# Optimization experiments

Measured on AMD Instinct MI355X. Metric: run time of the kernel, lower is better.

The kernel has to match this reference:

```python
import jax, jax.numpy as jnp
import numpy as np

N = 100000       # nodes
E = 1600000      # edges (avg degree 16)
F_IN = 128       # num_features
H = 128          # hidden
C = 10           # num_classes
L = 3            # num_layers
G = 128          # number of graphs in the batch


def setup_inputs() -> dict:
    key = jax.random.key(0)
    ks = jax.random.split(key, 12)
    x = jax.random.normal(ks[0], (N, F_IN), dtype=jnp.float32)
    edge_index = jax.random.randint(ks[1], (2, E), 0, N, dtype=jnp.int64)
    batch = jnp.sort(jax.random.randint(ks[2], (N,), 0, G, dtype=jnp.int64))
    def lin(k, fan_in, fan_out):
        s = 1.0 / np.sqrt(fan_in)
        return jax.random.uniform(k, (fan_in, fan_out), jnp.float32, -s, s)
    w_init = lin(ks[3], F_IN, H)
    b_init = jnp.zeros((H,), jnp.float32)
    w_conv = jnp.stack([lin(ks[4 + i], H, H) for i in range(L - 1)])  # [L-1,H,H]
    b_conv = jnp.zeros((L - 1, H), jnp.float32)
    w_h1 = lin(ks[8], H, H)
    b_h1 = jnp.zeros((H,), jnp.float32)
    w_h2 = lin(ks[9], H, C)
    b_h2 = jnp.zeros((C,), jnp.float32)
    return {"x": x, "edge_index": edge_index, "batch": batch,
            "w_init": w_init, "b_init": b_init,
            "w_conv": w_conv, "b_conv": b_conv,
            "w_h1": w_h1, "b_h1": b_h1, "w_h2": w_h2, "b_h2": b_h2}


def reference(x, edge_index, batch, w_init, b_init, w_conv, b_conv,
              w_h1, b_h1, w_h2, b_h2):
    n = x.shape[0]
    # GCNConv normalization: add self-loops, symmetric deg^-1/2 norm.
    loop = jnp.arange(n, dtype=edge_index.dtype)
    src = jnp.concatenate([edge_index[0], loop])
    dst = jnp.concatenate([edge_index[1], loop])
    deg = jax.ops.segment_sum(jnp.ones_like(dst, x.dtype), dst, num_segments=n)
    dinv = jnp.where(deg > 0, jax.lax.rsqrt(deg), 0.0)
    norm = dinv[src] * dinv[dst]  # [E+N]

    def gcn_conv(h, w, b):
        h = h @ w                                   # [N,H]
        msg = norm[:, None] * h[src]                # gather + scale
        return jax.ops.segment_sum(msg, dst, num_segments=n) + b

    h = jax.nn.relu(gcn_conv(x, w_init, b_init))
    for i in range(w_conv.shape[0]):
        h = jax.nn.relu(gcn_conv(h, w_conv[i], b_conv[i]))

    # global_mean_pool over graph ids
    sums = jax.ops.segment_sum(h, batch, num_segments=G)           # [G,H]
    cnt = jax.ops.segment_sum(jnp.ones((n,), h.dtype), batch, num_segments=G)
    pooled = sums / jnp.maximum(cnt, 1.0)[:, None]

    # classification head (dropout = identity at inference)
    h = jax.nn.relu(pooled @ w_h1 + b_h1)
    logits = h @ w_h2 + b_h2
    return jax.nn.log_softmax(logits, axis=-1)
```

## Files before the change

kernel.cpp:

```cpp
#include <hip/hip_runtime.h>
#include <hip/hip_bf16.h>
#include <math.h>

#define NN 100000
#define EE 1600000
#define HD 128
#define GG 128
#define CC 10

#define BKSH 9
#define NBK  196
#define CH   4096
#define MAXB 12288

typedef __attribute__((ext_vector_type(8))) short short8;
typedef __attribute__((ext_vector_type(4))) float f32x4;
typedef __attribute__((ext_vector_type(2))) float f32x2;

__device__ __forceinline__ unsigned short f2bf(float f) {
    union { float f; unsigned u; } a; a.f = f;
    unsigned r = a.u + 0x7fff + ((a.u >> 16) & 1);
    return (unsigned short)(r >> 16);
}
__device__ __forceinline__ float bfu(unsigned short u) {
    union { unsigned u; float f; } a; a.u = ((unsigned)u) << 16; return a.f;
}

__device__ __forceinline__ unsigned pk4fp8(float f0, float f1, float f2, float f3) {
    unsigned u = 0;
    u = __builtin_amdgcn_cvt_pk_fp8_f32(f0, f1, u, false);
    u = __builtin_amdgcn_cvt_pk_fp8_f32(f2, f3, u, true);
    return u;
}


__global__ __launch_bounds__(256) void k_bhist(const int* __restrict__ dst,
                                               unsigned* __restrict__ bucket_cnt) {
    __shared__ unsigned cnt[256];
    int t = threadIdx.x;
    cnt[t] = 0;
    __syncthreads();
    int base = blockIdx.x * CH;
#pragma unroll
    for (int k = 0; k < 16; ++k) {
        int e = base + k * 256 + t;
        if (e < EE) atomicAdd(&cnt[((unsigned)dst[e]) >> BKSH], 1u);
    }
    __syncthreads();
    if (cnt[t]) atomicAdd(&bucket_cnt[t], cnt[t]);
}

__global__ void k_bscan(const unsigned* __restrict__ bucket_cnt,
                        unsigned* __restrict__ bucket_start,
                        unsigned* __restrict__ cursor, int* __restrict__ row_start) {
    __shared__ unsigned s[256];
    int t = threadIdx.x;
    unsigned v = bucket_cnt[t];
    s[t] = v;
    __syncthreads();
    for (int off = 1; off < 256; off <<= 1) {
        unsigned a = (t >= off) ? s[t - off] : 0;
        __syncthreads();
        s[t] += a;
        __syncthreads();
    }
    unsigned excl = s[t] - v;
    bucket_start[t] = excl;
    cursor[t] = excl;
    if (t == 255) bucket_start[256] = excl + v;
    if (t == 0) row_start[NN] = EE;
}

__global__ __launch_bounds__(256) void k_bscatter(const int* __restrict__ src,
                                                  const int* __restrict__ dst,
                                                  unsigned* __restrict__ cursor,
                                                  unsigned* __restrict__ ebuf) {
    __shared__ unsigned cnt[256], lst[256], gbase[256], ss[256];
    __shared__ unsigned stage[CH];
    __shared__ unsigned char binid[CH];
    int t = threadIdx.x;
    cnt[t] = 0;
    __syncthreads();
    int base = blockIdx.x * CH;
    int nvalid = EE - base; if (nvalid > CH) nvalid = CH;

    unsigned bk[16], rk[16], pv[16];
#pragma unroll
    for (int k = 0; k < 16; ++k) {
        int e = base + k * 256 + t;
        bk[k] = 0xffffffffu;
        if (e < EE) {
            unsigned d = (unsigned)dst[e];
            unsigned b = d >> BKSH;
            pv[k] = (((unsigned)src[e]) << BKSH) | (d & ((1u << BKSH) - 1));
            bk[k] = b;
            rk[k] = atomicAdd(&cnt[b], 1u);
        }
    }
    __syncthreads();
    unsigned v = cnt[t];
    ss[t] = v;
    __syncthreads();
    for (int off = 1; off < 256; off <<= 1) {
        unsigned a = (t >= off) ? ss[t - off] : 0;
        __syncthreads();
        ss[t] += a;
        __syncthreads();
    }
    lst[t] = ss[t] - v;
    if (v) gbase[t] = atomicAdd(&cursor[t], v);
    __syncthreads();
#pragma unroll
    for (int k = 0; k < 16; ++k) {
        if (bk[k] != 0xffffffffu) {
            unsigned slot = lst[bk[k]] + rk[k];
            stage[slot] = pv[k];
            binid[slot] = (unsigned char)bk[k];
        }
    }
    __syncthreads();
    for (int j = t; j < nvalid; j += 256) {
        unsigned b = binid[j];
        ebuf[gbase[b] + (j - lst[b])] = stage[j];
    }
}

__global__ __launch_bounds__(512) void k_bucket_csr(const unsigned* __restrict__ ebuf,
                                                    const unsigned* __restrict__ bucket_start,
                                                    int* __restrict__ row_start,
                                                    float* __restrict__ dinv,
                                                    int* __restrict__ col) {
    __shared__ unsigned degl[512], lst[512], lfill[512], ss[512];
    __shared__ int colstage[MAXB];
    int t = threadIdx.x, b = blockIdx.x;
    unsigned ebase = bucket_start[b];
    int size = (int)(bucket_start[b + 1] - ebase);
    int nbase = b << BKSH;
    degl[t] = 0;
    lfill[t] = 0;
    __syncthreads();
    for (int j = t; j < size; j += 512)
        atomicAdd(&degl[ebuf[ebase + j] & 511u], 1u);
    __syncthreads();
    unsigned v = degl[t];
    ss[t] = v;
    __syncthreads();
    for (int off = 1; off < 512; off <<= 1) {
        unsigned a = (t >= off) ? ss[t - off] : 0;
        __syncthreads();
        ss[t] += a;
        __syncthreads();
    }
    lst[t] = ss[t] - v;
    int node = nbase + t;
    if (node < NN) {
        row_start[node] = (int)(ebase + lst[t]);
        dinv[node] = rsqrtf((float)(v + 1));
    }
    __syncthreads();
    if (size <= MAXB) {
        for (int j = t; j < size; j += 512) {
            unsigned u = ebuf[ebase + j];
            unsigned l = u & 511u;
            unsigned pos = lst[l] + atomicAdd(&lfill[l], 1u);
            colstage[pos] = (int)(u >> BKSH);
        }
        __syncthreads();
        for (int j = t; j < size; j += 512) col[ebase + j] = colstage[j];
    } else {
        for (int j = t; j < size; j += 512) {
            unsigned u = ebuf[ebase + j];
            unsigned l = u & 511u;
            unsigned pos = lst[l] + atomicAdd(&lfill[l], 1u);
            col[ebase + pos] = (int)(u >> BKSH);
        }
    }
}


__global__ void k_prep_w(const float* __restrict__ w0, const float* __restrict__ w1,
                         const float* __restrict__ w2, unsigned short* __restrict__ Wt) {
    int b = blockIdx.x;
    int mat = b >> 6;
    int idx = (b & 63) * 256 + threadIdx.x;
    int k = idx >> 7, n = idx & 127;
    const float* Wm = (mat == 0) ? w0 : ((mat == 1) ? w1 : w2);
    Wt[mat * 16384 + n * 128 + k] = f2bf(Wm[k * 128 + n]);
}


#define LDK 136

template <bool F32IN>
__global__ __launch_bounds__(256) void k_gemm_mfma(
    const void* __restrict__ Ap, const unsigned short* __restrict__ Wt,
    const float* __restrict__ dinv, unsigned* __restrict__ g8) {
    __shared__ unsigned short As[128 * LDK];
    __shared__ unsigned short Ws[128 * LDK];
    __shared__ float dv[128];
    int t = threadIdx.x;
    int r0 = blockIdx.x * 128;

#pragma unroll
    for (int p = 0; p < 8; ++p) {
        int chunk = p * 256 + t;
        int row = chunk >> 4, kc = chunk & 15;
        uint4 sv = make_uint4(0u, 0u, 0u, 0u);
        if (F32IN) {
            const float* A = (const float*)Ap;
            if (r0 + row < NN) {
                const float* ap = A + (size_t)(r0 + row) * HD + kc * 8;
                float4 va = *(const float4*)ap;
                float4 vb = *(const float4*)(ap + 4);
                sv.x = (unsigned)f2bf(va.x) | ((unsigned)f2bf(va.y) << 16);
                sv.y = (unsigned)f2bf(va.z) | ((unsigned)f2bf(va.w) << 16);
                sv.z = (unsigned)f2bf(vb.x) | ((unsigned)f2bf(vb.y) << 16);
                sv.w = (unsigned)f2bf(vb.z) | ((unsigned)f2bf(vb.w) << 16);
            }
        } else {
            const unsigned short* A = (const unsigned short*)Ap;
            if (r0 + row < NN) sv = *(const uint4*)(A + (size_t)(r0 + row) * HD + kc * 8);
        }
        *(uint4*)(As + row * LDK + kc * 8) = sv;
        uint4 w = *(const uint4*)(Wt + (size_t)row * HD + kc * 8);
        *(uint4*)(Ws + row * LDK + kc * 8) = w;
    }
    if (t < 128) dv[t] = (r0 + t < NN) ? dinv[r0 + t] : 0.f;
    __syncthreads();

    int wave = t >> 6, lane = t & 63, quad = lane >> 4, l16 = lane & 15;
    int wr = (wave >> 1) * 64, wc = (wave & 1) * 64;

    f32x4 acc[4][4];
#pragma unroll
    for (int i = 0; i < 4; ++i)
#pragma unroll
        for (int j = 0; j < 4; ++j) acc[i][j] = (f32x4){0.f, 0.f, 0.f, 0.f};

#pragma unroll
    for (int kk = 0; kk < 4; ++kk) {
        int k0 = kk * 32 + quad * 8;
        short8 af[4], bfr[4];
#pragma unroll
        for (int i = 0; i < 4; ++i)
            af[i] = *(const short8*)(As + (wr + i * 16 + l16) * LDK + k0);
#pragma unroll
        for (int j = 0; j < 4; ++j)
            bfr[j] = *(const short8*)(Ws + (wc + j * 16 + l16) * LDK + k0);
#pragma unroll
        for (int i = 0; i < 4; ++i)
#pragma unroll
            for (int j = 0; j < 4; ++j)
                acc[i][j] = __builtin_amdgcn_mfma_f32_16x16x32_bf16(af[i], bfr[j], acc[i][j], 0, 0, 0);
    }
    __syncthreads();

#pragma unroll
    for (int i = 0; i < 4; ++i) {
        int lr = wr + i * 16 + quad * 4;
#pragma unroll
        for (int reg = 0; reg < 4; ++reg) {
            float sc = dv[lr + reg];
#pragma unroll
            for (int j = 0; j < 4; ++j)
                As[(lr + reg) * LDK + wc + j * 16 + l16] = f2bf(acc[i][j][reg] * sc);
        }
    }
    __syncthreads();

    int row = t >> 1, half = t & 1;
    if (r0 + row < NN) {
        const unsigned short* sp = As + row * LDK + half * 64;
        unsigned og[16];
#pragma unroll
        for (int q = 0; q < 16; ++q)
            og[q] = pk4fp8(bfu(sp[4 * q]), bfu(sp[4 * q + 1]),
                           bfu(sp[4 * q + 2]), bfu(sp[4 * q + 3]));
        uint4* dp = (uint4*)(g8 + (size_t)(r0 + row) * 32 + half * 16);
#pragma unroll
        for (int q = 0; q < 4; ++q)
            dp[q] = make_uint4(og[4 * q], og[4 * q + 1], og[4 * q + 2], og[4 * q + 3]);
    }
}


__global__ __launch_bounds__(256) void k_aggregate(
    const unsigned* __restrict__ g8, const int* __restrict__ row_start,
    const int* __restrict__ col, const float* __restrict__ dinv,
    const float* __restrict__ bias, uint2* __restrict__ out) {
    int node = blockIdx.x * 8 + (threadIdx.x >> 5);
    int l = threadIdx.x & 31;
    unsigned su = g8[node * 32 + l];
    f32x2 slo = __builtin_amdgcn_cvt_pk_f32_fp8(su, false);
    f32x2 shi = __builtin_amdgcn_cvt_pk_f32_fp8(su, true);
    float a0 = slo.x, a1 = slo.y, a2 = shi.x, a3 = shi.y;
    int e = row_start[node], end = row_start[node + 1];
    for (; e + 8 <= end; e += 8) {
        int s0 = col[e], s1 = col[e + 1], s2 = col[e + 2], s3 = col[e + 3];
        int s4 = col[e + 4], s5 = col[e + 5], s6 = col[e + 6], s7 = col[e + 7];
        unsigned u0 = g8[s0 * 32 + l];
        unsigned u1 = g8[s1 * 32 + l];
        unsigned u2 = g8[s2 * 32 + l];
        unsigned u3 = g8[s3 * 32 + l];
        unsigned u4 = g8[s4 * 32 + l];
        unsigned u5 = g8[s5 * 32 + l];
        unsigned u6 = g8[s6 * 32 + l];
        unsigned u7 = g8[s7 * 32 + l];
#pragma unroll
        for (int k = 0; k < 8; ++k) {
            unsigned u = (k == 0) ? u0 : (k == 1) ? u1 : (k == 2) ? u2 : (k == 3) ? u3
                       : (k == 4) ? u4 : (k == 5) ? u5 : (k == 6) ? u6 : u7;
            f32x2 lo = __builtin_amdgcn_cvt_pk_f32_fp8(u, false);
            f32x2 hi = __builtin_amdgcn_cvt_pk_f32_fp8(u, true);
            a0 += lo.x; a1 += lo.y; a2 += hi.x; a3 += hi.y;
        }
    }
    for (; e < end; ++e) {
        unsigned u = g8[col[e] * 32 + l];
        f32x2 lo = __builtin_amdgcn_cvt_pk_f32_fp8(u, false);
        f32x2 hi = __builtin_amdgcn_cvt_pk_f32_fp8(u, true);
        a0 += lo.x; a1 += lo.y; a2 += hi.x; a3 += hi.y;
    }
    float sc = dinv[node];
    float4 bb = ((const float4*)bias)[l];
    float r0 = fmaxf(fmaf(a0, sc, bb.x), 0.f);
    float r1 = fmaxf(fmaf(a1, sc, bb.y), 0.f);
    float r2 = fmaxf(fmaf(a2, sc, bb.z), 0.f);
    float r3 = fmaxf(fmaf(a3, sc, bb.w), 0.f);
    uint2 o;
    o.x = (unsigned)f2bf(r0) | ((unsigned)f2bf(r1) << 16);
    o.y = (unsigned)f2bf(r2) | ((unsigned)f2bf(r3) << 16);
    out[node * 32 + l] = o;
}


__global__ __launch_bounds__(256) void k_pool_partial(
    const unsigned short* __restrict__ h, const int* __restrict__ batch,
    float* __restrict__ pooled, float* __restrict__ cntg) {
    int t = threadIdx.x;
    int slot = t >> 7, feat = t & 127;
    int base = blockIdx.x * 128;
    int endr = base + 128; if (endr > NN) endr = NN;
    float acc = 0.f;
    int cur = -1, run = 0;
    for (int r = base + slot; r < endr; r += 2) {
        int g = batch[r];
        float v = bfu(h[(size_t)r * HD + feat]);
        if (g != cur) {
            if (cur >= 0) {
                atomicAdd(&pooled[cur * HD + feat], acc);
                if (feat == 0) atomicAdd(&cntg[cur], (float)run);
            }
            cur = g; acc = 0.f; run = 0;
        }
        acc += v; ++run;
    }
    if (cur >= 0) {
        atomicAdd(&pooled[cur * HD + feat], acc);
        if (feat == 0) atomicAdd(&cntg[cur], (float)run);
    }
}


__global__ __launch_bounds__(128) void k_head(const float* __restrict__ pooled,
                                              const float* __restrict__ cntg,
                                              const float* __restrict__ w1,
                                              const float* __restrict__ b1,
                                              const float* __restrict__ w2,
                                              const float* __restrict__ b2,
                                              float* __restrict__ out) {
    __shared__ float row[HD], hrow[HD], logits[CC];
    int g = blockIdx.x, t = threadIdx.x;
    row[t] = pooled[g * HD + t] / fmaxf(cntg[g], 1.f);
    __syncthreads();
    float acc = b1[t];
    for (int k = 0; k < HD; ++k) acc = fmaf(row[k], w1[k * HD + t], acc);
    hrow[t] = fmaxf(acc, 0.f);
    __syncthreads();
    if (t < CC) {
        float a = b2[t];
        for (int k = 0; k < HD; ++k) a = fmaf(hrow[k], w2[k * CC + t], a);
        logits[t] = a;
    }
    __syncthreads();
    if (t < CC) {
        float m = logits[0];
        for (int i = 1; i < CC; ++i) m = fmaxf(m, logits[i]);
        float s = 0.f;
        for (int i = 0; i < CC; ++i) s += expf(logits[i] - m);
        out[g * CC + t] = logits[t] - m - logf(s);
    }
}


extern "C" void kernel_launch(void* const* d_in, const int* in_sizes, int n_in,
                              void* d_out, int out_size, void* d_ws, size_t ws_size,
                              hipStream_t stream) {
    const float* x      = (const float*)d_in[0];
    const int*   ei     = (const int*)d_in[1];
    const int*   batch  = (const int*)d_in[2];
    const float* w_init = (const float*)d_in[3];
    const float* b_init = (const float*)d_in[4];
    const float* w_conv = (const float*)d_in[5];
    const float* b_conv = (const float*)d_in[6];
    const float* w_h1   = (const float*)d_in[7];
    const float* b_h1   = (const float*)d_in[8];
    const float* w_h2   = (const float*)d_in[9];
    const float* b_h2   = (const float*)d_in[10];
    float* out = (float*)d_out;
    (void)n_in; (void)in_sizes; (void)out_size; (void)ws_size;

    char* ws = (char*)d_ws;
    size_t off = 0;
    auto alloc = [&](size_t bytes) -> void* {
        void* p = ws + off;
        off += (bytes + 255) & ~(size_t)255;
        return p;
    };
    unsigned short* hAbf         = (unsigned short*)alloc((size_t)NN * HD * 2);
    unsigned*       g8           = (unsigned*)alloc((size_t)NN * 32 * 4);
    unsigned short* Wt           = (unsigned short*)alloc(3 * 16384 * 2);
    float*          dinv         = (float*)alloc((size_t)NN * 4);
    int*            row_start    = (int*)alloc((size_t)(NN + 1) * 4);
    int*            col          = (int*)alloc((size_t)EE * 4);
    unsigned*       ebuf         = (unsigned*)alloc((size_t)EE * 4);
    unsigned*       bucket_cnt   = (unsigned*)alloc(256 * 4);
    unsigned*       bucket_start = (unsigned*)alloc(257 * 4);
    unsigned*       cursor       = (unsigned*)alloc(256 * 4);
    float*          pooled       = (float*)alloc((size_t)GG * HD * 4);
    float*          cntg         = (float*)alloc((size_t)GG * 4);

    const int* srcp = ei;
    const int* dstp = ei + EE;

    hipMemsetAsync(bucket_cnt, 0, 256 * 4, stream);
    hipMemsetAsync(pooled, 0, (size_t)GG * HD * 4, stream);
    hipMemsetAsync(cntg, 0, (size_t)GG * 4, stream);

    int nchunks = (EE + CH - 1) / CH;
    k_bhist<<<nchunks, 256, 0, stream>>>(dstp, bucket_cnt);
    k_bscan<<<1, 256, 0, stream>>>(bucket_cnt, bucket_start, cursor, row_start);
    k_bscatter<<<nchunks, 256, 0, stream>>>(srcp, dstp, cursor, ebuf);
    k_bucket_csr<<<NBK, 512, 0, stream>>>(ebuf, bucket_start, row_start, dinv, col);

    k_prep_w<<<192, 256, 0, stream>>>(w_init, w_conv, w_conv + HD * HD, Wt);

    int gemm_grid = (NN + 127) / 128;
    int agg_grid = NN / 8;

    k_gemm_mfma<true><<<gemm_grid, 256, 0, stream>>>(x, Wt, dinv, g8);
    k_aggregate<<<agg_grid, 256, 0, stream>>>(g8, row_start, col, dinv, b_init, (uint2*)hAbf);
    k_gemm_mfma<false><<<gemm_grid, 256, 0, stream>>>(hAbf, Wt + 16384, dinv, g8);
    k_aggregate<<<agg_grid, 256, 0, stream>>>(g8, row_start, col, dinv, b_conv, (uint2*)hAbf);
    k_gemm_mfma<false><<<gemm_grid, 256, 0, stream>>>(hAbf, Wt + 2 * 16384, dinv, g8);
    k_aggregate<<<agg_grid, 256, 0, stream>>>(g8, row_start, col, dinv, b_conv + HD, (uint2*)hAbf);

    k_pool_partial<<<(NN + 127) / 128, 256, 0, stream>>>(hAbf, batch, pooled, cntg);
    k_head<<<GG, 128, 0, stream>>>(pooled, cntg, w_h1, b_h1, w_h2, b_h2, out);
}
```

Before: 379.5 us.

## Fuse aggregation with next layer's GEMM and replace memsets with init kernel

Result: slower. 428.0 us (+12.8%).

```diff
diff --git a/kernel.cpp b/kernel.cpp
--- a/kernel.cpp
+++ b/kernel.cpp
@@ -31,6 +31,16 @@
     u = __builtin_amdgcn_cvt_pk_fp8_f32(f0, f1, u, false);
     u = __builtin_amdgcn_cvt_pk_fp8_f32(f2, f3, u, true);
     return u;
+}
+
+
+__global__ __launch_bounds__(256) void k_init(unsigned* __restrict__ bucket_cnt,
+                                              float* __restrict__ pooled,
+                                              float* __restrict__ cntg) {
+    int t = threadIdx.x;
+    bucket_cnt[t] = 0;
+    for (int i = t; i < GG * HD; i += 256) pooled[i] = 0.f;
+    if (t < GG) cntg[t] = 0.f;
 }
 
 
@@ -191,9 +201,8 @@
 
 #define LDK 136
 
-template <bool F32IN>
 __global__ __launch_bounds__(256) void k_gemm_mfma(
-    const void* __restrict__ Ap, const unsigned short* __restrict__ Wt,
+    const float* __restrict__ A, const unsigned short* __restrict__ Wt,
     const float* __restrict__ dinv, unsigned* __restrict__ g8) {
     __shared__ unsigned short As[128 * LDK];
     __shared__ unsigned short Ws[128 * LDK];
@@ -206,20 +215,14 @@
         int chunk = p * 256 + t;
         int row = chunk >> 4, kc = chunk & 15;
         uint4 sv = make_uint4(0u, 0u, 0u, 0u);
-        if (F32IN) {
-            const float* A = (const float*)Ap;
-            if (r0 + row < NN) {
-                const float* ap = A + (size_t)(r0 + row) * HD + kc * 8;
-                float4 va = *(const float4*)ap;
-                float4 vb = *(const float4*)(ap + 4);
-                sv.x = (unsigned)f2bf(va.x) | ((unsigned)f2bf(va.y) << 16);
-                sv.y = (unsigned)f2bf(va.z) | ((unsigned)f2bf(va.w) << 16);
-                sv.z = (unsigned)f2bf(vb.x) | ((unsigned)f2bf(vb.y) << 16);
-                sv.w = (unsigned)f2bf(vb.z) | ((unsigned)f2bf(vb.w) << 16);
-            }
-        } else {
-            const unsigned short* A = (const unsigned short*)Ap;
-            if (r0 + row < NN) sv = *(const uint4*)(A + (size_t)(r0 + row) * HD + kc * 8);
+        if (r0 + row < NN) {
+            const float* ap = A + (size_t)(r0 + row) * HD + kc * 8;
+            float4 va = *(const float4*)ap;
+            float4 vb = *(const float4*)(ap + 4);
+            sv.x = (unsigned)f2bf(va.x) | ((unsigned)f2bf(va.y) << 16);
+            sv.y = (unsigned)f2bf(va.z) | ((unsigned)f2bf(va.w) << 16);
+            sv.z = (unsigned)f2bf(vb.x) | ((unsigned)f2bf(vb.y) << 16);
+            sv.w = (unsigned)f2bf(vb.z) | ((unsigned)f2bf(vb.w) << 16);
         }
         *(uint4*)(As + row * LDK + kc * 8) = sv;
         uint4 w = *(const uint4*)(Wt + (size_t)row * HD + kc * 8);
@@ -280,6 +283,116 @@
 #pragma unroll
         for (int q = 0; q < 4; ++q)
             dp[q] = make_uint4(og[4 * q], og[4 * q + 1], og[4 * q + 2], og[4 * q + 3]);
+    }
+}
+
+
+__global__ __launch_bounds__(256) void k_agg_gemm(
+    const unsigned* __restrict__ g8in, const int* __restrict__ row_start,
+    const int* __restrict__ col, const float* __restrict__ dinv,
+    const float* __restrict__ bias, const unsigned short* __restrict__ Wt,
+    unsigned* __restrict__ g8out) {
+    __shared__ unsigned short As[64 * LDK];
+    __shared__ float dv[64];
+    int t = threadIdx.x;
+    int r0 = blockIdx.x * 64;
+    if (t < 64) dv[t] = (r0 + t < NN) ? dinv[r0 + t] : 0.f;
+
+    int h = t >> 5, l = t & 31;
+    float4 bb = ((const float4*)bias)[l];
+
+    for (int p = 0; p < 8; ++p) {
+        int row = h * 8 + p;
+        int node = r0 + row;
+        unsigned lo_u = 0, hi_u = 0;
+        if (node < NN) {
+            unsigned su = g8in[node * 32 + l];
+            f32x2 a01 = __builtin_amdgcn_cvt_pk_f32_fp8(su, false);
+            f32x2 a23 = __builtin_amdgcn_cvt_pk_f32_fp8(su, true);
+            int e = row_start[node], end = row_start[node + 1];
+            for (; e + 8 <= end; e += 8) {
+                int s0 = col[e], s1 = col[e + 1], s2 = col[e + 2], s3 = col[e + 3];
+                int s4 = col[e + 4], s5 = col[e + 5], s6 = col[e + 6], s7 = col[e + 7];
+                unsigned u0 = g8in[s0 * 32 + l];
+                unsigned u1 = g8in[s1 * 32 + l];
+                unsigned u2 = g8in[s2 * 32 + l];
+                unsigned u3 = g8in[s3 * 32 + l];
+                unsigned u4 = g8in[s4 * 32 + l];
+                unsigned u5 = g8in[s5 * 32 + l];
+                unsigned u6 = g8in[s6 * 32 + l];
+                unsigned u7 = g8in[s7 * 32 + l];
+#pragma unroll
+                for (int k = 0; k < 8; ++k) {
+                    unsigned u = (k == 0) ? u0 : (k == 1) ? u1 : (k == 2) ? u2 : (k == 3) ? u3
+                               : (k == 4) ? u4 : (k == 5) ? u5 : (k == 6) ? u6 : u7;
+                    a01 += __builtin_amdgcn_cvt_pk_f32_fp8(u, false);
+                    a23 += __builtin_amdgcn_cvt_pk_f32_fp8(u, true);
+                }
+            }
+            for (; e < end; ++e) {
+                unsigned u = g8in[col[e] * 32 + l];
+                a01 += __builtin_amdgcn_cvt_pk_f32_fp8(u, false);
+                a23 += __builtin_amdgcn_cvt_pk_f32_fp8(u, true);
+            }
+            float sc = dinv[node];
+            float r0f = fmaxf(fmaf(a01.x, sc, bb.x), 0.f);
+            float r1f = fmaxf(fmaf(a01.y, sc, bb.y), 0.f);
+            float r2f = fmaxf(fmaf(a23.x, sc, bb.z), 0.f);
+            float r3f = fmaxf(fmaf(a23.y, sc, bb.w), 0.f);
+            lo_u = (unsigned)f2bf(r0f) | ((unsigned)f2bf(r1f) << 16);
+            hi_u = (unsigned)f2bf(r2f) | ((unsigned)f2bf(r3f) << 16);
+        }
+        *(uint2*)(As + row * LDK + 4 * l) = make_uint2(lo_u, hi_u);
+    }
+    __syncthreads();
+
+    int wave = t >> 6, lane = t & 63, quad = lane >> 4, l16 = lane & 15;
+    f32x4 acc[4][2];
+#pragma unroll
+    for (int i = 0; i < 4; ++i)
+#pragma unroll
+        for (int j = 0; j < 2; ++j) acc[i][j] = (f32x4){0.f, 0.f, 0.f, 0.f};
+
+#pragma unroll
+    for (int kk = 0; kk < 4; ++kk) {
+        int k0 = kk * 32 + quad * 8;
+        short8 af[4];
+#pragma unroll
+        for (int i = 0; i < 4; ++i)
+            af[i] = *(const short8*)(As + (i * 16 + l16) * LDK + k0);
+        short8 b0 = *(const short8*)(Wt + (size_t)(wave * 32 + l16) * HD + k0);
+        short8 b1 = *(const short8*)(Wt + (size_t)(wave * 32 + 16 + l16) * HD + k0);
+#pragma unroll
+        for (int i = 0; i < 4; ++i) {
+            acc[i][0] = __builtin_amdgcn_mfma_f32_16x16x32_bf16(af[i], b0, acc[i][0], 0, 0, 0);
+            acc[i][1] = __builtin_amdgcn_mfma_f32_16x16x32_bf16(af[i], b1, acc[i][1], 0, 0, 0);
+        }
+    }
+    __syncthreads();
+
+#pragma unroll
+    for (int i = 0; i < 4; ++i) {
+        int lr = i * 16 + quad * 4;
+#pragma unroll
+        for (int reg = 0; reg < 4; ++reg) {
+            float sc = dv[lr + reg];
+            As[(lr + reg) * LDK + wave * 32 + l16] = f2bf(acc[i][0][reg] * sc);
+            As[(lr + reg) * LDK + wave * 32 + 16 + l16] = f2bf(acc[i][1][reg] * sc);
+        }
+    }
+    __syncthreads();
+
+    int row = t >> 2, seg = t & 3;
+    if (r0 + row < NN) {
+        const unsigned short* sp = As + row * LDK + seg * 32;
+        unsigned og[8];
+#pragma unroll
+        for (int q = 0; q < 8; ++q)
+            og[q] = pk4fp8(bfu(sp[4 * q]), bfu(sp[4 * q + 1]),
+                           bfu(sp[4 * q + 2]), bfu(sp[4 * q + 3]));
+        uint4* dp = (uint4*)(g8out + (size_t)(r0 + row) * 32 + seg * 8);
+        dp[0] = make_uint4(og[0], og[1], og[2], og[3]);
+        dp[1] = make_uint4(og[4], og[5], og[6], og[7]);
     }
 }
 
@@ -418,7 +531,8 @@
         return p;
     };
     unsigned short* hAbf         = (unsigned short*)alloc((size_t)NN * HD * 2);
-    unsigned*       g8           = (unsigned*)alloc((size_t)NN * 32 * 4);
+    unsigned*       g8a          = (unsigned*)alloc((size_t)NN * 32 * 4);
+    unsigned*       g8b          = (unsigned*)alloc((size_t)NN * 32 * 4);
     unsigned short* Wt           = (unsigned short*)alloc(3 * 16384 * 2);
     float*          dinv         = (float*)alloc((size_t)NN * 4);
     int*            row_start    = (int*)alloc((size_t)(NN + 1) * 4);
@@ -433,9 +547,7 @@
     const int* srcp = ei;
     const int* dstp = ei + EE;
 
-    hipMemsetAsync(bucket_cnt, 0, 256 * 4, stream);
-    hipMemsetAsync(pooled, 0, (size_t)GG * HD * 4, stream);
-    hipMemsetAsync(cntg, 0, (size_t)GG * 4, stream);
+    k_init<<<1, 256, 0, stream>>>(bucket_cnt, pooled, cntg);
 
     int nchunks = (EE + CH - 1) / CH;
     k_bhist<<<nchunks, 256, 0, stream>>>(dstp, bucket_cnt);
@@ -446,14 +558,13 @@
     k_prep_w<<<192, 256, 0, stream>>>(w_init, w_conv, w_conv + HD * HD, Wt);
 
     int gemm_grid = (NN + 127) / 128;
+    int fuse_grid = (NN + 63) / 64;
     int agg_grid = NN / 8;
 
-    k_gemm_mfma<true><<<gemm_grid, 256, 0, stream>>>(x, Wt, dinv, g8);
-    k_aggregate<<<agg_grid, 256, 0, stream>>>(g8, row_start, col, dinv, b_init, (uint2*)hAbf);
-    k_gemm_mfma<false><<<gemm_grid, 256, 0, stream>>>(hAbf, Wt + 16384, dinv, g8);
-    k_aggregate<<<agg_grid, 256, 0, stream>>>(g8, row_start, col, dinv, b_conv, (uint2*)hAbf);
-    k_gemm_mfma<false><<<gemm_grid, 256, 0, stream>>>(hAbf, Wt + 2 * 16384, dinv, g8);
-    k_aggregate<<<agg_grid, 256, 0, stream>>>(g8, row_start, col, dinv, b_conv + HD, (uint2*)hAbf);
+    k_gemm_mfma<<<gemm_grid, 256, 0, stream>>>(x, Wt, dinv, g8a);
+    k_agg_gemm<<<fuse_grid, 256, 0, stream>>>(g8a, row_start, col, dinv, b_init, Wt + 16384, g8b);
+    k_agg_gemm<<<fuse_grid, 256, 0, stream>>>(g8b, row_start, col, dinv, b_conv, Wt + 2 * 16384, g8a);
+    k_aggregate<<<agg_grid, 256, 0, stream>>>(g8a, row_start, col, dinv, b_conv + HD, (uint2*)hAbf);
 
     k_pool_partial<<<(NN + 127) / 128, 256, 0, stream>>>(hAbf, batch, pooled, cntg);
     k_head<<<GG, 128, 0, stream>>>(pooled, cntg, w_h1, b_h1, w_h2, b_h2, out);
```

## Use full wave per node in aggregation with bpermute-broadcast neighbor indices

Applied to the files above, without the earlier changes.

Result: slower. 389.8 us (+2.7%).

```diff
diff --git a/kernel.cpp b/kernel.cpp
--- a/kernel.cpp
+++ b/kernel.cpp
@@ -125,50 +125,52 @@
     }
 }
 
-__global__ __launch_bounds__(512) void k_bucket_csr(const unsigned* __restrict__ ebuf,
-                                                    const unsigned* __restrict__ bucket_start,
-                                                    int* __restrict__ row_start,
-                                                    float* __restrict__ dinv,
-                                                    int* __restrict__ col) {
+__global__ __launch_bounds__(1024) void k_bucket_csr(const unsigned* __restrict__ ebuf,
+                                                     const unsigned* __restrict__ bucket_start,
+                                                     int* __restrict__ row_start,
+                                                     float* __restrict__ dinv,
+                                                     int* __restrict__ col) {
     __shared__ unsigned degl[512], lst[512], lfill[512], ss[512];
     __shared__ int colstage[MAXB];
     int t = threadIdx.x, b = blockIdx.x;
     unsigned ebase = bucket_start[b];
     int size = (int)(bucket_start[b + 1] - ebase);
     int nbase = b << BKSH;
-    degl[t] = 0;
-    lfill[t] = 0;
-    __syncthreads();
-    for (int j = t; j < size; j += 512)
+    if (t < 512) { degl[t] = 0; lfill[t] = 0; }
+    __syncthreads();
+    for (int j = t; j < size; j += 1024)
         atomicAdd(&degl[ebuf[ebase + j] & 511u], 1u);
     __syncthreads();
-    unsigned v = degl[t];
-    ss[t] = v;
+    unsigned v = 0;
+    if (t < 512) { v = degl[t]; ss[t] = v; }
     __syncthreads();
     for (int off = 1; off < 512; off <<= 1) {
-        unsigned a = (t >= off) ? ss[t - off] : 0;
-        __syncthreads();
-        ss[t] += a;
-        __syncthreads();
-    }
-    lst[t] = ss[t] - v;
-    int node = nbase + t;
-    if (node < NN) {
-        row_start[node] = (int)(ebase + lst[t]);
-        dinv[node] = rsqrtf((float)(v + 1));
+        unsigned a = 0;
+        if (t < 512 && t >= off) a = ss[t - off];
+        __syncthreads();
+        if (t < 512) ss[t] += a;
+        __syncthreads();
+    }
+    if (t < 512) {
+        lst[t] = ss[t] - v;
+        int node = nbase + t;
+        if (node < NN) {
+            row_start[node] = (int)(ebase + lst[t]);
+            dinv[node] = rsqrtf((float)(v + 1));
+        }
     }
     __syncthreads();
     if (size <= MAXB) {
-        for (int j = t; j < size; j += 512) {
+        for (int j = t; j < size; j += 1024) {
             unsigned u = ebuf[ebase + j];
             unsigned l = u & 511u;
             unsigned pos = lst[l] + atomicAdd(&lfill[l], 1u);
             colstage[pos] = (int)(u >> BKSH);
         }
         __syncthreads();
-        for (int j = t; j < size; j += 512) col[ebase + j] = colstage[j];
+        for (int j = t; j < size; j += 1024) col[ebase + j] = colstage[j];
     } else {
-        for (int j = t; j < size; j += 512) {
+        for (int j = t; j < size; j += 1024) {
             unsigned u = ebuf[ebase + j];
             unsigned l = u & 511u;
             unsigned pos = lst[l] + atomicAdd(&lfill[l], 1u);
@@ -179,10 +181,19 @@
 
 
 __global__ void k_prep_w(const float* __restrict__ w0, const float* __restrict__ w1,
-                         const float* __restrict__ w2, unsigned short* __restrict__ Wt) {
+                         const float* __restrict__ w2, unsigned short* __restrict__ Wt,
+                         unsigned* __restrict__ bucket_cnt, float* __restrict__ pooled,
+                         float* __restrict__ cntg) {
     int b = blockIdx.x;
+    int t = threadIdx.x;
+    if (b == 192) {
+        bucket_cnt[t] = 0;
+        for (int i = t; i < GG * HD; i += 256) pooled[i] = 0.f;
+        if (t < GG) cntg[t] = 0.f;
+        return;
+    }
     int mat = b >> 6;
-    int idx = (b & 63) * 256 + threadIdx.x;
+    int idx = (b & 63) * 256 + t;
     int k = idx >> 7, n = idx & 127;
     const float* Wm = (mat == 0) ? w0 : ((mat == 1) ? w1 : w2);
     Wt[mat * 16384 + n * 128 + k] = f2bf(Wm[k * 128 + n]);
@@ -288,49 +299,65 @@
     const unsigned* __restrict__ g8, const int* __restrict__ row_start,
     const int* __restrict__ col, const float* __restrict__ dinv,
     const float* __restrict__ bias, uint2* __restrict__ out) {
-    int node = blockIdx.x * 8 + (threadIdx.x >> 5);
-    int l = threadIdx.x & 31;
-    unsigned su = g8[node * 32 + l];
-    f32x2 slo = __builtin_amdgcn_cvt_pk_f32_fp8(su, false);
-    f32x2 shi = __builtin_amdgcn_cvt_pk_f32_fp8(su, true);
-    float a0 = slo.x, a1 = slo.y, a2 = shi.x, a3 = shi.y;
+    int node = blockIdx.x * 4 + (threadIdx.x >> 6);
+    int lane = threadIdx.x & 63;
+    int half = lane >> 5, l32 = lane & 31;
+
+    f32x2 a01 = (f32x2){0.f, 0.f}, a23 = (f32x2){0.f, 0.f};
+    {
+        unsigned su = (half == 0) ? g8[node * 32 + l32] : 0u;
+        a01 += __builtin_amdgcn_cvt_pk_f32_fp8(su, false);
+        a23 += __builtin_amdgcn_cvt_pk_f32_fp8(su, true);
+    }
+
     int e = row_start[node], end = row_start[node + 1];
-    for (; e + 8 <= end; e += 8) {
-        int s0 = col[e], s1 = col[e + 1], s2 = col[e + 2], s3 = col[e + 3];
-        int s4 = col[e + 4], s5 = col[e + 5], s6 = col[e + 6], s7 = col[e + 7];
-        unsigned u0 = g8[s0 * 32 + l];
-        unsigned u1 = g8[s1 * 32 + l];
-        unsigned u2 = g8[s2 * 32 + l];
-        unsigned u3 = g8[s3 * 32 + l];
-        unsigned u4 = g8[s4 * 32 + l];
-        unsigned u5 = g8[s5 * 32 + l];
-        unsigned u6 = g8[s6 * 32 + l];
-        unsigned u7 = g8[s7 * 32 + l];
-#pragma unroll
-        for (int k = 0; k < 8; ++k) {
-            unsigned u = (k == 0) ? u0 : (k == 1) ? u1 : (k == 2) ? u2 : (k == 3) ? u3
-                       : (k == 4) ? u4 : (k == 5) ? u5 : (k == 6) ? u6 : u7;
-            f32x2 lo = __builtin_amdgcn_cvt_pk_f32_fp8(u, false);
-            f32x2 hi = __builtin_amdgcn_cvt_pk_f32_fp8(u, true);
-            a0 += lo.x; a1 += lo.y; a2 += hi.x; a3 += hi.y;
-        }
-    }
-    for (; e < end; ++e) {
-        unsigned u = g8[col[e] * 32 + l];
-        f32x2 lo = __builtin_amdgcn_cvt_pk_f32_fp8(u, false);
-        f32x2 hi = __builtin_amdgcn_cvt_pk_f32_fp8(u, true);
-        a0 += lo.x; a1 += lo.y; a2 += hi.x; a3 += hi.y;
-    }
-    float sc = dinv[node];
-    float4 bb = ((const float4*)bias)[l];
-    float r0 = fmaxf(fmaf(a0, sc, bb.x), 0.f);
-    float r1 = fmaxf(fmaf(a1, sc, bb.y), 0.f);
-    float r2 = fmaxf(fmaf(a2, sc, bb.z), 0.f);
-    float r3 = fmaxf(fmaf(a3, sc, bb.w), 0.f);
-    uint2 o;
-    o.x = (unsigned)f2bf(r0) | ((unsigned)f2bf(r1) << 16);
-    o.y = (unsigned)f2bf(r2) | ((unsigned)f2bf(r3) << 16);
-    out[node * 32 + l] = o;
+    while (e < end) {
+        int cnt = end - e; if (cnt > 64) cnt = 64;
+        int li = lane < cnt ? lane : cnt - 1;
+        int colv = col[e + li];
+        int k = 0;
+        for (; k + 16 <= cnt; k += 16) {
+            unsigned u[8];
+#pragma unroll
+            for (int q = 0; q < 8; ++q) {
+                int src = __builtin_amdgcn_ds_bpermute((k + q * 2 + half) << 2, colv);
+                u[q] = g8[(unsigned)src * 32 + l32];
+            }
+#pragma unroll
+            for (int q = 0; q < 8; ++q) {
+                a01 += __builtin_amdgcn_cvt_pk_f32_fp8(u[q], false);
+                a23 += __builtin_amdgcn_cvt_pk_f32_fp8(u[q], true);
+            }
+        }
+        for (; k < cnt; k += 2) {
+            int kk = k + half;
+            bool valid = kk < cnt;
+            int src = __builtin_amdgcn_ds_bpermute((valid ? kk : k) << 2, colv);
+            unsigned u = g8[(unsigned)src * 32 + l32];
+            if (!valid) u = 0u;
+            a01 += __builtin_amdgcn_cvt_pk_f32_fp8(u, false);
+            a23 += __builtin_amdgcn_cvt_pk_f32_fp8(u, true);
+        }
+        e += cnt;
+    }
+
+    a01.x += __shfl_down(a01.x, 32);
+    a01.y += __shfl_down(a01.y, 32);
+    a23.x += __shfl_down(a23.x, 32);
+    a23.y += __shfl_down(a23.y, 32);
+
+    if (half == 0) {
+        float sc = dinv[node];
+        float4 bb = ((const float4*)bias)[l32];
+        float r0 = fmaxf(fmaf(a01.x, sc, bb.x), 0.f);
+        float r1 = fmaxf(fmaf(a01.y, sc, bb.y), 0.f);
+        float r2 = fmaxf(fmaf(a23.x, sc, bb.z), 0.f);
+        float r3 = fmaxf(fmaf(a23.y, sc, bb.w), 0.f);
+        uint2 o;
+        o.x = (unsigned)f2bf(r0) | ((unsigned)f2bf(r1) << 16);
+        o.y = (unsigned)f2bf(r2) | ((unsigned)f2bf(r3) << 16);
+        out[node * 32 + l32] = o;
+    }
 }
 
 
@@ -433,20 +460,17 @@
     const int* srcp = ei;
     const int* dstp = ei + EE;
 
-    hipMemsetAsync(bucket_cnt, 0, 256 * 4, stream);
-    hipMemsetAsync(pooled, 0, (size_t)GG * HD * 4, stream);
-    hipMemsetAsync(cntg, 0, (size_t)GG * 4, stream);
+    k_prep_w<<<193, 256, 0, stream>>>(w_init, w_conv, w_conv + HD * HD, Wt,
+                                      bucket_cnt, pooled, cntg);
 
     int nchunks = (EE + CH - 1) / CH;
     k_bhist<<<nchunks, 256, 0, stream>>>(dstp, bucket_cnt);
     k_bscan<<<1, 256, 0, stream>>>(bucket_cnt, bucket_start, cursor, row_start);
     k_bscatter<<<nchunks, 256, 0, stream>>>(srcp, dstp, cursor, ebuf);
-    k_bucket_csr<<<NBK, 512, 0, stream>>>(ebuf, bucket_start, row_start, dinv, col);
-
-    k_prep_w<<<192, 256, 0, stream>>>(w_init, w_conv, w_conv + HD * HD, Wt);
+    k_bucket_csr<<<NBK, 1024, 0, stream>>>(ebuf, bucket_start, row_start, dinv, col);
 
     int gemm_grid = (NN + 127) / 128;
-    int agg_grid = NN / 8;
+    int agg_grid = NN / 4;
 
     k_gemm_mfma<true><<<gemm_grid, 256, 0, stream>>>(x, Wt, dinv, g8);
     k_aggregate<<<agg_grid, 256, 0, stream>>>(g8, row_start, col, dinv, b_init, (uint2*)hAbf);
```
